# Kernel optimization log

Measured on AMD Instinct MI355X. Metric: run time of the kernel, lower is better.

## Reference

```python
import jax, jax.numpy as jnp
import numpy as np

EPS = 1e-12  # F.normalize default eps


def setup_inputs() -> dict:
    key = jax.random.key(0)
    x = jax.random.normal(key, (10000, 512), dtype=jnp.float32)
    return {"x": x, "k": 9}


def reference(x, k):
    # F.normalize(x, p=2, dim=0): L2-normalize each feature column over points
    col_norm = jnp.sqrt(jnp.sum(x * x, axis=0, keepdims=True))  # [1, D]
    xn = x / jnp.maximum(col_norm, EPS)                          # [N, D]

    # pairwise squared euclidean distance: ||xi||^2 - 2 xi.xj + ||xj||^2
    sq = jnp.sum(xn * xn, axis=-1, keepdims=True)                # [N, 1]
    dist = sq - 2.0 * (xn @ xn.T) + sq.T                          # [N, N]

    # k nearest neighbors = top-k of negative distance
    _, nn_idx = jax.lax.top_k(-dist, k)                           # [N, k] int32

    n = x.shape[0]
    center_idx = jnp.broadcast_to(jnp.arange(n, dtype=nn_idx.dtype)[:, None], (n, k))
    edge_idx = jnp.stack((nn_idx, center_idx), axis=0)            # [2, N, k]
    return edge_idx
```

## Files before the change

kernel.cpp:

```cpp
#include <hip/hip_runtime.h>
#include <hip/hip_cooperative_groups.h>
#include <math.h>

namespace cg = cooperative_groups;

#define DD 512
#define NBLKA 400

#define PM 128
#define PN 256
#define KB 32
#define CSPLIT 6
#define NC 12
#define PBUF 32
#define PBSTRIDE 36
#define NCTOT (CSPLIT*NC)
#define KOUTMAX 16
#define RS_MARGIN 2e-4f

typedef __attribute__((ext_vector_type(8))) short bf16x8;
typedef __attribute__((ext_vector_type(4))) float f32x4;

static __device__ __forceinline__ unsigned short f2bf(float f) {
    unsigned u = __float_as_uint(f);
    u += 0x7fff + ((u >> 16) & 1);
    return (unsigned short)(u >> 16);
}

__global__ __launch_bounds__(256) void prekernel(
    const float* __restrict__ x, double* __restrict__ partial,
    double* __restrict__ rn, double* __restrict__ w,
    double* __restrict__ sq, float* __restrict__ sqf,
    unsigned short* __restrict__ xnbf, int N, int rows_per_block, int nblk)
{
    cg::grid_group grid = cg::this_grid();
    const int t = threadIdx.x;

    {
        int b  = blockIdx.x;
        int r0 = b * rows_per_block;
        int r1 = min(r0 + rows_per_block, N);
        double s0 = 0.0, s1 = 0.0;
        for (int r = r0; r < r1; ++r) {
            float v0 = x[(size_t)r * DD + t];
            float v1 = x[(size_t)r * DD + t + 256];
            s0 += (double)v0 * (double)v0;
            s1 += (double)v1 * (double)v1;
        }
        partial[(size_t)b * DD + t]       = s0;
        partial[(size_t)b * DD + t + 256] = s1;
    }
    grid.sync();

    __shared__ double red[256];
    if (blockIdx.x < 256) {
#pragma unroll 1
        for (int cc = 0; cc < 2; ++cc) {
            int c = blockIdx.x * 2 + cc;
            double s = 0.0;
            for (int b = t; b < nblk; b += 256) s += partial[(size_t)b * DD + c];
            red[t] = s;
            __syncthreads();
            for (int off = 128; off > 0; off >>= 1) {
                if (t < off) red[t] += red[t + off];
                __syncthreads();
            }
            if (t == 0) {
                double n = fmax(sqrt(red[0]), 1e-12);
                double r = 1.0 / n;
                rn[c] = r;
                w[c]  = r * r;
            }
            __syncthreads();
        }
    }
    grid.sync();

    {
        int lane   = t & 63;
        int gwave  = (blockIdx.x * blockDim.x + t) >> 6;
        int nwaves = (gridDim.x * blockDim.x) >> 6;
        const double2* rp = (const double2*)rn;
        double2 r0a = rp[lane * 2],       r0b = rp[lane * 2 + 1];
        double2 r1a = rp[128 + lane * 2], r1b = rp[128 + lane * 2 + 1];
        for (int i = gwave; i < N; i += nwaves) {
            const float4* xr = (const float4*)(x + (size_t)i * DD);
            float4 v0 = xr[lane];
            float4 v1 = xr[64 + lane];
            double a0 = (double)v0.x * r0a.x, a1 = (double)v0.y * r0a.y;
            double a2 = (double)v0.z * r0b.x, a3 = (double)v0.w * r0b.y;
            double b0 = (double)v1.x * r1a.x, b1 = (double)v1.y * r1a.y;
            double b2 = (double)v1.z * r1b.x, b3 = (double)v1.w * r1b.y;
            ushort4 s0 = { f2bf((float)a0), f2bf((float)a1), f2bf((float)a2), f2bf((float)a3) };
            ushort4 s1 = { f2bf((float)b0), f2bf((float)b1), f2bf((float)b2), f2bf((float)b3) };
            *(ushort4*)(xnbf + (size_t)i * DD + lane * 4)       = s0;
            *(ushort4*)(xnbf + (size_t)i * DD + 256 + lane * 4) = s1;
            double loc = a0*a0 + a1*a1 + a2*a2 + a3*a3 + b0*b0 + b1*b1 + b2*b2 + b3*b3;
#pragma unroll
            for (int off = 32; off > 0; off >>= 1)
                loc += __shfl_xor(loc, off, 64);
            if (lane == 0) { sq[i] = loc; sqf[i] = (float)loc; }
        }
    }
}

__global__ __launch_bounds__(256, 2) void gemm_prefilter(
    const unsigned short* __restrict__ xnbf,
    const float* __restrict__ sqf, int* __restrict__ cand, float* __restrict__ cands,
    int N, int ntileM, int ntileN)
{
    __shared__ __align__(16) unsigned char lds_raw[49152];
    __shared__ float sqi_s[PM];
    __shared__ float sqj_s[PN];
    __shared__ float thr_s[PM];
    __shared__ int   cnt_s[PM];
    __shared__ int   flag_s;

    float (*Bsc)[PBSTRIDE] = (float (*)[PBSTRIDE]) lds_raw;
    int   (*Bid)[PBSTRIDE] = (int   (*)[PBSTRIDE]) (lds_raw + 24576);

    const int bid   = blockIdx.x;
    const int q     = bid & 7;
    const int s     = bid >> 3;
    const int ridx  = s / CSPLIT;
    const int split = s - ridx * CSPLIT;
    const int rowb  = q + 8 * ridx;
    if (rowb >= ntileM) return;
    const int row0  = rowb * PM;

    const int t      = threadIdx.x;
    const int lane15 = t & 15;
    const int quad   = (t >> 4) & 3;
    const int wave   = t >> 6;
    const int wr     = (wave >> 1) * 64;
    const int wc     = (wave & 1) * 128;
    const int sl     = quad ^ (lane15 & 3);

    if (t == 0) flag_s = 0;
    if (t < PM) {
        int i = row0 + t;
        sqi_s[t] = (i < N) ? sqf[i] : 0.f;
        thr_s[t] = __builtin_inff();
        cnt_s[t] = 0;
    }

    float ls[NC];
    int   li[NC];
#pragma unroll
    for (int m = 0; m < NC; ++m) { ls[m] = __builtin_inff(); li[m] = 0x7fffffff; }

    f32x4 acc[4][8];

    for (int tile = split; tile < ntileN; tile += CSPLIT) {
        int col0 = tile * PN;

        {
            int j = col0 + t;
            sqj_s[t] = (j < N) ? sqf[j] : __builtin_inff();
        }
        __syncthreads();

#pragma unroll
        for (int mt = 0; mt < 4; ++mt)
#pragma unroll
            for (int nt = 0; nt < 8; ++nt)
                acc[mt][nt] = (f32x4){0.f, 0.f, 0.f, 0.f};

        auto STAGE = [&](int kc, int buf) {
            unsigned char* base = lds_raw + (size_t)buf * 24576;
#pragma unroll
            for (int l = 0; l < 2; ++l) {
                int e   = t + l * 256;
                int row = e >> 2;
                int c   = (e & 3) ^ (row & 3);
                size_t g = (size_t)(row0 + row) * DD + kc + c * 8;
                __builtin_amdgcn_global_load_lds(
                    (const unsigned int*)(xnbf + g),
                    (unsigned int*)(base + (size_t)e * 16), 16, 0, 0);
            }
#pragma unroll
            for (int l = 0; l < 4; ++l) {
                int e   = t + l * 256;
                int row = e >> 2;
                int c   = (e & 3) ^ (row & 3);
                size_t g = (size_t)(col0 + row) * DD + kc + c * 8;
                __builtin_amdgcn_global_load_lds(
                    (const unsigned int*)(xnbf + g),
                    (unsigned int*)(base + 8192 + (size_t)e * 16), 16, 0, 0);
            }
        };

        STAGE(0, 0);
#pragma unroll 1
        for (int cc = 0; cc < 16; ++cc) {
            if (cc < 15) {
                STAGE((cc + 1) * KB, (cc + 1) & 1);
                __builtin_amdgcn_sched_barrier(0);
                asm volatile("s_waitcnt vmcnt(6)" ::: "memory");
            } else {
                __builtin_amdgcn_sched_barrier(0);
                asm volatile("s_waitcnt vmcnt(0)" ::: "memory");
            }
            __builtin_amdgcn_s_barrier();
            __builtin_amdgcn_sched_barrier(0);

            const unsigned char* rb = lds_raw + (size_t)(cc & 1) * 24576;
            bf16x8 af[4], bfg[8];
#pragma unroll
            for (int mt = 0; mt < 4; ++mt)
                af[mt] = *(const bf16x8*)(rb + (size_t)(wr + mt * 16 + lane15) * 64 + sl * 16);
#pragma unroll
            for (int nt = 0; nt < 8; ++nt)
                bfg[nt] = *(const bf16x8*)(rb + 8192 + (size_t)(wc + nt * 16 + lane15) * 64 + sl * 16);
#pragma unroll
            for (int mt = 0; mt < 4; ++mt)
#pragma unroll
                for (int nt = 0; nt < 8; ++nt)
                    acc[mt][nt] = __builtin_amdgcn_mfma_f32_16x16x32_bf16(
                        af[mt], bfg[nt], acc[mt][nt], 0, 0, 0);
            __builtin_amdgcn_sched_barrier(0);
            __builtin_amdgcn_s_barrier();
        }

#pragma unroll
        for (int mt = 0; mt < 4; ++mt)
#pragma unroll
            for (int nt = 0; nt < 8; ++nt)
#pragma unroll
                for (int reg = 0; reg < 4; ++reg) {
                    int rl = wr + mt * 16 + quad * 4 + reg;
                    int cl = wc + nt * 16 + lane15;
                    float g = acc[mt][nt][reg];
                    acc[mt][nt][reg] = (sqi_s[rl] - 2.f * g) + sqj_s[cl];
                }
        __syncthreads();

        auto MERGE = [&]() {
            if (t < PM) {
                int c = cnt_s[t];
                if (c > PBUF) c = PBUF;
                cnt_s[t] = 0;
                for (int m0 = 0; m0 < c; m0 += 4) {
                    float4 s4 = *(const float4*)&Bsc[t][m0];
                    int4   j4 = *(const int4*)&Bid[t][m0];
#pragma unroll
                    for (int e = 0; e < 4; ++e) {
                        if (m0 + e >= c) break;
                        float sv = (e == 0) ? s4.x : (e == 1) ? s4.y : (e == 2) ? s4.z : s4.w;
                        int   j  = (e == 0) ? j4.x : (e == 1) ? j4.y : (e == 2) ? j4.z : j4.w;
                        if (sv < ls[NC - 1] || (sv == ls[NC - 1] && j < li[NC - 1])) {
                            float cs = sv; int cj = j;
#pragma unroll
                            for (int p = 0; p < NC; ++p) {
                                bool lt = (cs < ls[p]) || (cs == ls[p] && cj < li[p]);
                                float ts = ls[p]; int tj = li[p];
                                if (lt) { ls[p] = cs; li[p] = cj; cs = ts; cj = tj; }
                            }
                        }
                    }
                }
                thr_s[t] = ls[NC - 1];
            }
        };

        bool tile_edge = (col0 + PN > N);
        unsigned long long done0 = 0ull, done1 = 0ull;

        if (tile == split) {
#pragma unroll
            for (int mt = 0; mt < 4; ++mt)
#pragma unroll
                for (int reg = 0; reg < 4; ++reg) {
                    int rl = wr + mt * 16 + quad * 4 + reg;
                    float mn = __builtin_inff(); int bn = -1;
#pragma unroll
                    for (int nt = 0; nt < 8; ++nt) {
                        float sv = acc[mt][nt][reg];
                        int   j  = col0 + wc + nt * 16 + lane15;
                        if (j < N && sv < mn) { mn = sv; bn = nt; }
                    }
                    if (bn >= 0) {
                        int pos = atomicAdd(&cnt_s[rl], 1);
                        if (pos < PBUF) {
                            Bsc[rl][pos] = mn;
                            Bid[rl][pos] = col0 + wc + bn * 16 + lane15;
                            unsigned long long bit =
                                1ull << (mt * 16 + (bn & 3) * 4 + reg);
                            if (bn < 4) done0 |= bit; else done1 |= bit;
                        }
                    } else {
                        unsigned long long gb = (0x1111ull << reg) << (mt * 16);
                        done0 |= gb; done1 |= gb;
                    }
                }
            __syncthreads();
            MERGE();
            __syncthreads();
        }

        for (;;) {
#pragma unroll
            for (int hn = 0; hn < 2; ++hn) {
#pragma unroll
                for (int mt = 0; mt < 4; ++mt)
#pragma unroll
                    for (int reg = 0; reg < 4; ++reg) {
                        const unsigned long long gb =
                            (0x1111ull << reg) << (mt * 16);
                        unsigned long long dn = hn ? done1 : done0;
                        int rl = wr + mt * 16 + quad * 4 + reg;
                        float th = thr_s[rl];
                        float gmin = fminf(
                            fminf(acc[mt][hn * 4 + 0][reg], acc[mt][hn * 4 + 1][reg]),
                            fminf(acc[mt][hn * 4 + 2][reg], acc[mt][hn * 4 + 3][reg]));
                        if (!tile_edge && gmin > th) {
                            if (hn) done1 |= gb; else done0 |= gb;
                            continue;
                        }
                        if ((dn & gb) == gb) continue;
#pragma unroll
                        for (int u = 0; u < 4; ++u) {
                            const unsigned long long bit = 1ull << (mt * 16 + u * 4 + reg);
                            if (!(dn & bit)) {
                                float sv = acc[mt][hn * 4 + u][reg];
                                int   j  = col0 + wc + (hn * 4 + u) * 16 + lane15;
                                bool ok = false;
                                if (j < N && sv <= th) {
                                    int pos = atomicAdd(&cnt_s[rl], 1);
                                    if (pos < PBUF) {
                                        Bsc[rl][pos] = sv;
                                        Bid[rl][pos] = j;
                                        ok = true;
                                    }
                                } else {
                                    ok = true;
                                }
                                if (ok) { if (hn) done1 |= bit; else done0 |= bit; }
                            }
                        }
                    }
            }
            if (done0 != ~0ull || done1 != ~0ull) flag_s = 1;
            __syncthreads();
            MERGE();
            __syncthreads();
            int go = flag_s;
            __syncthreads();
            if (t == 0) flag_s = 0;
            __syncthreads();
            if (!go) break;
        }
    }
    if (t < PM) {
        int i = row0 + t;
        if (i < N) {
#pragma unroll
            for (int m = 0; m < NC; ++m) {
                cand [(size_t)i * NCTOT + split * NC + m] = li[m];
                cands[(size_t)i * NCTOT + split * NC + m] = ls[m];
            }
        }
    }
}

__global__ __launch_bounds__(256) void rescore_topk(
    const float* __restrict__ x, const double* __restrict__ w,
    const double* __restrict__ sq, const int* __restrict__ cand,
    const float* __restrict__ cands, int* __restrict__ out, int N, int k)
{
    __shared__ float Ssc[4][NCTOT];
    int lane = threadIdx.x & 63;
    int wid  = threadIdx.x >> 6;
    int i = blockIdx.x * 4 + wid;
    if (i >= N) return;

    size_t base = (size_t)i * NCTOT;
    Ssc[wid][lane] = cands[base + lane];
    if (lane < NCTOT - 64) Ssc[wid][64 + lane] = cands[base + 64 + lane];

    float p0 = Ssc[wid][lane];
    float p1 = Ssc[wid][64 + (lane & 7)];
    int c0 = 0, c1 = 0;
    for (int m = 0; m < NCTOT; ++m) {
        float s = Ssc[wid][m];
        c0 += (s <= p0); c1 += (s <= p1);
    }
    float best = __builtin_inff();
    if (c0 >= k) best = p0;
    if (c1 >= k && p1 < best) best = p1;
#pragma unroll
    for (int off = 32; off > 0; off >>= 1)
        best = fminf(best, __shfl_xor(best, off, 64));
    float cut = best + RS_MARGIN;

    double aw[8];
#pragma unroll
    for (int c = 0; c < 8; ++c) {
        int d = lane + 64 * c;
        aw[c] = (double)x[(size_t)i * DD + d] * w[d];
    }
    double sqi = sq[i];

    double bs[KOUTMAX];
    int    bj[KOUTMAX];
    for (int r = 0; r < k; ++r) { bs[r] = __builtin_inf(); bj[r] = 0x7fffffff; }

    int pend = -1;
    for (int m = 0; m <= NCTOT; ++m) {
        int j1cand = -1;
        if (m < NCTOT) {
            if (Ssc[wid][m] > cut) continue;
            j1cand = cand[base + m];
            if (pend < 0) { pend = j1cand; continue; }
        } else if (pend < 0) {
            break;
        }
        int j0 = pend, j1 = j1cand;
        pend = -1;
        const float* q0 = &x[(size_t)j0 * DD + lane];
        const float* q1 = (j1 >= 0) ? &x[(size_t)j1 * DD + lane] : q0;
        float v0[8], v1[8];
#pragma unroll
        for (int c = 0; c < 8; ++c) v0[c] = q0[64 * c];
#pragma unroll
        for (int c = 0; c < 8; ++c) v1[c] = q1[64 * c];
        double d0 = 0.0, d1 = 0.0;
#pragma unroll
        for (int c = 0; c < 8; ++c) d0 = fma(aw[c], (double)v0[c], d0);
#pragma unroll
        for (int c = 0; c < 8; ++c) d1 = fma(aw[c], (double)v1[c], d1);
#pragma unroll
        for (int off = 32; off > 0; off >>= 1) {
            d0 += __shfl_xor(d0, off, 64);
            d1 += __shfl_xor(d1, off, 64);
        }
        double s0 = (sqi - 2.0 * d0) + sq[j0];
        double s1 = (j1 >= 0) ? (sqi - 2.0 * d1) + sq[j1] : __builtin_inf();
#pragma unroll 1
        for (int pick = 0; pick < 2; ++pick) {
            double sv = pick ? s1 : s0;
            int    j  = pick ? j1 : j0;
            if (j < 0) continue;
            if (sv < bs[k - 1] || (sv == bs[k - 1] && j < bj[k - 1])) {
                int pos = k - 1;
                while (pos > 0) {
                    double ps = bs[pos - 1]; int pj = bj[pos - 1];
                    if (!(sv < ps || (sv == ps && j < pj))) break;
                    bs[pos] = ps; bj[pos] = pj;
                    --pos;
                }
                bs[pos] = sv; bj[pos] = j;
            }
        }
    }
    if (lane == 0) {
        for (int r = 0; r < k; ++r) {
            out[(size_t)i * k + r]                 = bj[r];
            out[(size_t)N * k + (size_t)i * k + r] = i;
        }
    }
}

extern "C" void kernel_launch(void* const* d_in, const int* in_sizes, int n_in,
                              void* d_out, int out_size, void* d_ws, size_t ws_size,
                              hipStream_t stream) {
    const float* x = (const float*)d_in[0];
    int N = in_sizes[0] / DD;
    int k = out_size / (2 * N);
    if (k > KOUTMAX) k = KOUTMAX;

    char* ws = (char*)d_ws;
    double*         partial = (double*)ws;
    double*         rn      = (double*)(ws + 1638400);
    double*         w       = (double*)(ws + 1642496);
    double*         sq      = (double*)(ws + 1646592);
    float*          sqf     = (float*) (ws + 1726592);
    unsigned short* xnbf    = (unsigned short*)(ws + 1766592);
    int*            cand    = (int*)   (ws + 12006592);
    float*          cands   = (float*) (ws + 14886592);

    int rpb  = (N + NBLKA - 1) / NBLKA;
    int nblk = NBLKA;
    void* pre_args[] = { (void*)&x, (void*)&partial, (void*)&rn, (void*)&w,
                         (void*)&sq, (void*)&sqf, (void*)&xnbf,
                         (void*)&N, (void*)&rpb, (void*)&nblk };
    hipLaunchCooperativeKernel((const void*)prekernel, dim3(NBLKA), dim3(256),
                               pre_args, 0, stream);

    int ntileM = (N + PM - 1) / PM;
    int ntileN = (N + PN - 1) / PN;
    int rows_per_xcd = (ntileM + 7) / 8;
    int nblkc = 8 * rows_per_xcd * CSPLIT;
    hipLaunchKernelGGL(gemm_prefilter, dim3(nblkc), dim3(256), 0, stream,
                       xnbf, sqf, cand, cands, N, ntileM, ntileN);

    hipLaunchKernelGGL(rescore_topk, dim3((N + 3) / 4), dim3(256), 0, stream,
                       x, w, sq, cand, cands, (int*)d_out, N, k);
}
```

Measured before the change: 669.9 us.

## Pre-tile bf16 normalized matrix into swizzled LDS-ready blocks for GEMM staging

The prekernel now writes the bf16 normalized rows into two tiled buffers (128-row A tiles and 256-row B tiles, split into 32-wide K chunks with the XOR swizzle already applied), padded with zeros. The GEMM's global_load_lds staging then reads each chunk as one contiguous linear block instead of strided 64-byte row pieces. The aim is fully coalesced, contiguous loads and less address arithmetic in the hot loop. The cost is writing the matrix twice, using more workspace, and scattered 8-byte stores in the prekernel.

```diff
diff --git a/kernel.cpp b/kernel.cpp
--- a/kernel.cpp
+++ b/kernel.cpp
@@ -31,7 +31,8 @@
     const float* __restrict__ x, double* __restrict__ partial,
     double* __restrict__ rn, double* __restrict__ w,
     double* __restrict__ sq, float* __restrict__ sqf,
-    unsigned short* __restrict__ xnbf, int N, int rows_per_block, int nblk)
+    unsigned char* __restrict__ Atiled, unsigned char* __restrict__ Btiled,
+    int N, int rows_per_block, int nblk, int NpadA, int NpadB)
 {
     cg::grid_group grid = cg::this_grid();
     const int t = threadIdx.x;
@@ -83,29 +84,45 @@
         const double2* rp = (const double2*)rn;
         double2 r0a = rp[lane * 2],       r0b = rp[lane * 2 + 1];
         double2 r1a = rp[128 + lane * 2], r1b = rp[128 + lane * 2 + 1];
-        for (int i = gwave; i < N; i += nwaves) {
-            const float4* xr = (const float4*)(x + (size_t)i * DD);
-            float4 v0 = xr[lane];
-            float4 v1 = xr[64 + lane];
-            double a0 = (double)v0.x * r0a.x, a1 = (double)v0.y * r0a.y;
-            double a2 = (double)v0.z * r0b.x, a3 = (double)v0.w * r0b.y;
-            double b0 = (double)v1.x * r1a.x, b1 = (double)v1.y * r1a.y;
-            double b2 = (double)v1.z * r1b.x, b3 = (double)v1.w * r1b.y;
-            ushort4 s0 = { f2bf((float)a0), f2bf((float)a1), f2bf((float)a2), f2bf((float)a3) };
-            ushort4 s1 = { f2bf((float)b0), f2bf((float)b1), f2bf((float)b2), f2bf((float)b3) };
-            *(ushort4*)(xnbf + (size_t)i * DD + lane * 4)       = s0;
-            *(ushort4*)(xnbf + (size_t)i * DD + 256 + lane * 4) = s1;
-            double loc = a0*a0 + a1*a1 + a2*a2 + a3*a3 + b0*b0 + b1*b1 + b2*b2 + b3*b3;
-#pragma unroll
-            for (int off = 32; off > 0; off >>= 1)
-                loc += __shfl_xor(loc, off, 64);
-            if (lane == 0) { sq[i] = loc; sqf[i] = (float)loc; }
+        const int le0 = lane, le1 = lane + 64;
+        const int cc0 = le0 >> 3, gl0 = (le0 & 7) >> 1, hf0 = le0 & 1;
+        const int cc1 = le1 >> 3, gl1 = (le1 & 7) >> 1, hf1 = le1 & 1;
+        for (int i = gwave; i < NpadB; i += nwaves) {
+            ushort4 s0 = {0,0,0,0}, s1 = {0,0,0,0};
+            if (i < N) {
+                const float4* xr = (const float4*)(x + (size_t)i * DD);
+                float4 v0 = xr[lane];
+                float4 v1 = xr[64 + lane];
+                double a0 = (double)v0.x * r0a.x, a1 = (double)v0.y * r0a.y;
+                double a2 = (double)v0.z * r0b.x, a3 = (double)v0.w * r0b.y;
+                double b0 = (double)v1.x * r1a.x, b1 = (double)v1.y * r1a.y;
+                double b2 = (double)v1.z * r1b.x, b3 = (double)v1.w * r1b.y;
+                s0 = (ushort4){ f2bf((float)a0), f2bf((float)a1), f2bf((float)a2), f2bf((float)a3) };
+                s1 = (ushort4){ f2bf((float)b0), f2bf((float)b1), f2bf((float)b2), f2bf((float)b3) };
+                double loc = a0*a0 + a1*a1 + a2*a2 + a3*a3 + b0*b0 + b1*b1 + b2*b2 + b3*b3;
+#pragma unroll
+                for (int off = 32; off > 0; off >>= 1)
+                    loc += __shfl_xor(loc, off, 64);
+                if (lane == 0) { sq[i] = loc; sqf[i] = (float)loc; }
+            }
+            int sw = i & 3;
+            if (i < NpadA) {
+                size_t tb = ((size_t)(i >> 7) * 16) * 8192 + (size_t)(i & 127) * 64;
+                *(ushort4*)(Atiled + tb + (size_t)cc0 * 8192 + (gl0 ^ sw) * 16 + hf0 * 8) = s0;
+                *(ushort4*)(Atiled + tb + (size_t)cc1 * 8192 + (gl1 ^ sw) * 16 + hf1 * 8) = s1;
+            }
+            {
+                size_t tb = ((size_t)(i >> 8) * 16) * 16384 + (size_t)(i & 255) * 64;
+                *(ushort4*)(Btiled + tb + (size_t)cc0 * 16384 + (gl0 ^ sw) * 16 + hf0 * 8) = s0;
+                *(ushort4*)(Btiled + tb + (size_t)cc1 * 16384 + (gl1 ^ sw) * 16 + hf1 * 8) = s1;
+            }
         }
     }
 }
 
 __global__ __launch_bounds__(256, 2) void gemm_prefilter(
-    const unsigned short* __restrict__ xnbf,
+    const unsigned char* __restrict__ Atiled,
+    const unsigned char* __restrict__ Btiled,
     const float* __restrict__ sqf, int* __restrict__ cand, float* __restrict__ cands,
     int N, int ntileM, int ntileN)
 {
@@ -151,8 +168,11 @@
 
     f32x4 acc[4][8];
 
+    const unsigned char* Abase = Atiled + (size_t)rowb * 16 * 8192;
+
     for (int tile = split; tile < ntileN; tile += CSPLIT) {
         int col0 = tile * PN;
+        const unsigned char* Bbase = Btiled + (size_t)tile * 16 * 16384;
 
         {
             int j = col0 + t;
@@ -166,26 +186,22 @@
             for (int nt = 0; nt < 8; ++nt)
                 acc[mt][nt] = (f32x4){0.f, 0.f, 0.f, 0.f};
 
-        auto STAGE = [&](int kc, int buf) {
+        auto STAGE = [&](int cc, int buf) {
             unsigned char* base = lds_raw + (size_t)buf * 24576;
+            const unsigned char* sa = Abase + (size_t)cc * 8192;
+            const unsigned char* sb = Bbase + (size_t)cc * 16384;
 #pragma unroll
             for (int l = 0; l < 2; ++l) {
-                int e   = t + l * 256;
-                int row = e >> 2;
-                int c   = (e & 3) ^ (row & 3);
-                size_t g = (size_t)(row0 + row) * DD + kc + c * 8;
+                int e = t + l * 256;
                 __builtin_amdgcn_global_load_lds(
-                    (const unsigned int*)(xnbf + g),
+                    (const unsigned int*)(sa + (size_t)e * 16),
                     (unsigned int*)(base + (size_t)e * 16), 16, 0, 0);
             }
 #pragma unroll
             for (int l = 0; l < 4; ++l) {
-                int e   = t + l * 256;
-                int row = e >> 2;
-                int c   = (e & 3) ^ (row & 3);
-                size_t g = (size_t)(col0 + row) * DD + kc + c * 8;
+                int e = t + l * 256;
                 __builtin_amdgcn_global_load_lds(
-                    (const unsigned int*)(xnbf + g),
+                    (const unsigned int*)(sb + (size_t)e * 16),
                     (unsigned int*)(base + 8192 + (size_t)e * 16), 16, 0, 0);
             }
         };
@@ -194,7 +210,7 @@
 #pragma unroll 1
         for (int cc = 0; cc < 16; ++cc) {
             if (cc < 15) {
-                STAGE((cc + 1) * KB, (cc + 1) & 1);
+                STAGE(cc + 1, (cc + 1) & 1);
                 __builtin_amdgcn_sched_barrier(0);
                 asm volatile("s_waitcnt vmcnt(6)" ::: "memory");
             } else {
@@ -469,30 +485,35 @@
     int k = out_size / (2 * N);
     if (k > KOUTMAX) k = KOUTMAX;
 
+    int ntileM = (N + PM - 1) / PM;
+    int ntileN = (N + PN - 1) / PN;
+    int NpadA  = ntileM * PM;
+    int NpadB  = ntileN * PN;
+
     char* ws = (char*)d_ws;
-    double*         partial = (double*)ws;
-    double*         rn      = (double*)(ws + 1638400);
-    double*         w       = (double*)(ws + 1642496);
-    double*         sq      = (double*)(ws + 1646592);
-    float*          sqf     = (float*) (ws + 1726592);
-    unsigned short* xnbf    = (unsigned short*)(ws + 1766592);
-    int*            cand    = (int*)   (ws + 12006592);
-    float*          cands   = (float*) (ws + 14886592);
+    double*        partial = (double*)ws;
+    double*        rn      = (double*)(ws + 1638400);
+    double*        w       = (double*)(ws + 1642496);
+    double*        sq      = (double*)(ws + 1646592);
+    float*         sqf     = (float*) (ws + 1726592);
+    unsigned char* Atiled  = (unsigned char*)(ws + 1766592);
+    unsigned char* Btiled  = (unsigned char*)(ws + 12121280);
+    int*           cand    = (int*)   (ws + 22607040);
+    float*         cands   = (float*) (ws + 25487040);
 
     int rpb  = (N + NBLKA - 1) / NBLKA;
     int nblk = NBLKA;
     void* pre_args[] = { (void*)&x, (void*)&partial, (void*)&rn, (void*)&w,
-                         (void*)&sq, (void*)&sqf, (void*)&xnbf,
-                         (void*)&N, (void*)&rpb, (void*)&nblk };
+                         (void*)&sq, (void*)&sqf, (void*)&Atiled, (void*)&Btiled,
+                         (void*)&N, (void*)&rpb, (void*)&nblk,
+                         (void*)&NpadA, (void*)&NpadB };
     hipLaunchCooperativeKernel((const void*)prekernel, dim3(NBLKA), dim3(256),
                                pre_args, 0, stream);
 
-    int ntileM = (N + PM - 1) / PM;
-    int ntileN = (N + PN - 1) / PN;
     int rows_per_xcd = (ntileM + 7) / 8;
     int nblkc = 8 * rows_per_xcd * CSPLIT;
     hipLaunchKernelGGL(gemm_prefilter, dim3(nblkc), dim3(256), 0, stream,
-                       xnbf, sqf, cand, cands, N, ntileM, ntileN);
+                       Atiled, Btiled, sqf, cand, cands, N, ntileM, ntileN);
 
     hipLaunchKernelGGL(rescore_topk, dim3((N + 3) / 4), dim3(256), 0, stream,
                        x, w, sq, cand, cands, (int*)d_out, N, k);
```

Measured after the change: 666.8 us. Within noise of the previous version (-0.5%).
